# Performance work log

Hardware: AMD Instinct MI355X
Metric: run time of the kernel (lower is better)

## Reference

```python
import jax, jax.numpy as jnp
import numpy as np

B, O, L, T = 1024, 50, 20, 10
D, H, V = 64, 128, 49688
DM, FF = 2 * H, 4 * H  # transformer d_model=256, ffn=512


def _ln(x, g, b, eps=1e-5):
    m = x.mean(-1, keepdims=True)
    v = ((x - m) ** 2).mean(-1, keepdims=True)
    return (x - m) / jnp.sqrt(v + eps) * g + b


def _mha(x, in_w, in_b, out_w, out_b, nh):
    # x: [..., S, d]; torch nn.MultiheadAttention with packed qkv in_proj
    lead, S, d = x.shape[:-2], x.shape[-2], x.shape[-1]
    hd = d // nh
    qkv = x @ in_w.T + in_b
    q, k, v = jnp.split(qkv, 3, axis=-1)
    q = q.reshape(*lead, S, nh, hd)
    k = k.reshape(*lead, S, nh, hd)
    v = v.reshape(*lead, S, nh, hd)
    sc = jnp.einsum('...qhd,...khd->...hqk', q, k) / jnp.sqrt(jnp.asarray(hd, x.dtype))
    a = jax.nn.softmax(sc, axis=-1)
    o = jnp.einsum('...hqk,...khd->...qhd', a, v).reshape(*lead, S, d)
    return o @ out_w.T + out_b


def _gru_dir(x_seq, wi, wh, bi, bh):
    # x_seq: [O, B, D] -> outputs [O, B, H]; PyTorch GRU cell equations
    def step(h, x):
        gi = x @ wi.T + bi
        gh = h @ wh.T + bh
        i_r, i_z, i_n = jnp.split(gi, 3, axis=-1)
        h_r, h_z, h_n = jnp.split(gh, 3, axis=-1)
        r = jax.nn.sigmoid(i_r + h_r)
        z = jax.nn.sigmoid(i_z + h_z)
        n = jnp.tanh(i_n + r * h_n)
        h2 = (1.0 - z) * n + z * h
        return h2, h2
    h0 = jnp.zeros((x_seq.shape[1], wh.shape[1]), x_seq.dtype)
    _, ys = jax.lax.scan(step, h0, x_seq)
    return ys


def setup_inputs() -> dict:
    key = jax.random.key(0)
    ks = jax.random.split(key, 20)
    rn = lambda k, shape: jax.random.normal(k, shape, jnp.float32) * 0.05
    return {
        'order_history': jax.random.randint(ks[0], (B, O, L), 0, V, jnp.int32),
        'days_between': jax.random.uniform(ks[1], (B, T), jnp.float32) * 30.0,
        'days_since_last': jax.random.uniform(ks[2], (B,), jnp.float32) * 30.0,
        'item_emb': rn(ks[3], (V + 1, D)).at[0].set(0.0),  # padding_idx=0
        'ia_in_w': rn(ks[4], (3 * D, D)), 'ia_in_b': jnp.zeros(3 * D),
        'ia_out_w': rn(ks[5], (D, D)), 'ia_out_b': jnp.zeros(D),
        'gf_wi': rn(ks[6], (3 * H, D)), 'gf_wh': rn(ks[7], (3 * H, H)),
        'gf_bi': jnp.zeros(3 * H), 'gf_bh': jnp.zeros(3 * H),
        'gb_wi': rn(ks[8], (3 * H, D)), 'gb_wh': rn(ks[9], (3 * H, H)),
        'gb_bi': jnp.zeros(3 * H), 'gb_bh': jnp.zeros(3 * H),
        'ta_in_w': rn(ks[10], (3 * DM, DM)), 'ta_in_b': jnp.zeros(3 * DM),
        'ta_out_w': rn(ks[11], (DM, DM)), 'ta_out_b': jnp.zeros(DM),
        't_ln1_g': jnp.ones(DM), 't_ln1_b': jnp.zeros(DM),
        't_ln2_g': jnp.ones(DM), 't_ln2_b': jnp.zeros(DM),
        't_ff1_w': rn(ks[12], (FF, DM)), 't_ff1_b': jnp.zeros(FF),
        't_ff2_w': rn(ks[13], (DM, FF)), 't_ff2_b': jnp.zeros(DM),
        'te1_w': rn(ks[14], (H // 4, 2)), 'te1_b': jnp.zeros(H // 4),
        'te_ln1_g': jnp.ones(H // 4), 'te_ln1_b': jnp.zeros(H // 4),
        'te2_w': rn(ks[15], (H // 2, H // 4)), 'te2_b': jnp.zeros(H // 2),
        'te_ln2_g': jnp.ones(H // 2), 'te_ln2_b': jnp.zeros(H // 2),
        'c_w': rn(ks[16], (H, DM + H // 2)), 'c_b': jnp.zeros(H),
        'c_ln_g': jnp.ones(H), 'c_ln_b': jnp.zeros(H),
    }


def reference(order_history, days_between, days_since_last, item_emb,
              ia_in_w, ia_in_b, ia_out_w, ia_out_b,
              gf_wi, gf_wh, gf_bi, gf_bh, gb_wi, gb_wh, gb_bi, gb_bh,
              ta_in_w, ta_in_b, ta_out_w, ta_out_b,
              t_ln1_g, t_ln1_b, t_ln2_g, t_ln2_b,
              t_ff1_w, t_ff1_b, t_ff2_w, t_ff2_b,
              te1_w, te1_b, te_ln1_g, te_ln1_b, te2_w, te2_b, te_ln2_g, te_ln2_b,
              c_w, c_b, c_ln_g, c_ln_b):
    # per-order item embedding + self-attention + mean pool (batched over B,O)
    E = item_emb[order_history]                            # [B,O,L,D]
    A = _mha(E, ia_in_w, ia_in_b, ia_out_w, ia_out_b, 4)   # [B,O,L,D]
    order_emb = A.mean(axis=2)                             # [B,O,D]
    # bidirectional GRU over order sequence
    x = jnp.transpose(order_emb, (1, 0, 2))                # [O,B,D]
    yf = _gru_dir(x, gf_wi, gf_wh, gf_bi, gf_bh)
    yb = _gru_dir(x[::-1], gb_wi, gb_wh, gb_bi, gb_bh)[::-1]
    g = jnp.transpose(jnp.concatenate([yf, yb], axis=-1), (1, 0, 2))  # [B,O,2H]
    # post-norm TransformerEncoderLayer (dropout inactive at eval)
    sa = _mha(g, ta_in_w, ta_in_b, ta_out_w, ta_out_b, 4)
    h1 = _ln(g + sa, t_ln1_g, t_ln1_b)
    ff = jax.nn.relu(h1 @ t_ff1_w.T + t_ff1_b) @ t_ff2_w.T + t_ff2_b
    h2 = _ln(h1 + ff, t_ln2_g, t_ln2_b)
    order_enc = h2.mean(axis=1)                            # [B,2H]
    # temporal features: mean(days_between), recency (days_std is unused in original)
    feat = jnp.stack([days_between.mean(axis=1), days_since_last], axis=1)  # [B,2]
    t1 = jax.nn.relu(_ln(feat @ te1_w.T + te1_b, te_ln1_g, te_ln1_b))
    t2 = jax.nn.relu(_ln(t1 @ te2_w.T + te2_b, te_ln2_g, te_ln2_b))        # [B,H//2]
    u = jnp.concatenate([order_enc, t2], axis=1)           # [B,2H+H//2]
    return jax.nn.relu(_ln(u @ c_w.T + c_b, c_ln_g, c_ln_b))  # [B,H]
```

## Files before the change

### kernel.cpp

```cpp
#include <hip/hip_runtime.h>


#define B_ 1024
#define O_ 50
#define VROWS 49689
#define VPAD  49792

typedef __attribute__((ext_vector_type(8))) short  short8v;
typedef __attribute__((ext_vector_type(4))) short  short4v;
typedef __attribute__((ext_vector_type(8))) unsigned short ushort8v;
typedef __attribute__((ext_vector_type(4))) unsigned short ushort4v;
typedef __attribute__((ext_vector_type(4))) float f32x4;

__device__ __forceinline__ float sig_(float x)  { return 1.0f / (1.0f + __expf(-x)); }
__device__ __forceinline__ float tanh_(float x) { return 2.0f / (1.0f + __expf(-2.0f * x)) - 1.0f; }

__device__ __forceinline__ unsigned short f2bf(float f) {
  union { float f; unsigned int u; } v; v.f = f;
  unsigned int r = v.u + 0x7FFFu + ((v.u >> 16) & 1u);
  return (unsigned short)(r >> 16);
}
__device__ __forceinline__ float bf2f(unsigned short u) {
  union { unsigned int u; float f; } v; v.u = ((unsigned int)u) << 16;
  return v.f;
}
__device__ __forceinline__ unsigned int pk2bf(float lo, float hi) {
  return (unsigned int)f2bf(lo) | ((unsigned int)f2bf(hi) << 16);
}

struct CvArgs {
  const float* src[10];
  unsigned short* dst[10];
  int n[10];
};
__global__ void k_cv_multi(CvArgs a) {
  int i = blockIdx.x * 256 + threadIdx.x;
#pragma unroll
  for (int s = 0; s < 10; ++s) {
    if (i < a.n[s]) { a.dst[s][i] = f2bf(a.src[s][i]); return; }
    i -= a.n[s];
  }
}

__global__ void k_prep_small(const float* __restrict__ c_w, float* __restrict__ w_c,
                             const float* __restrict__ bia, const float* __restrict__ bib,
                             float* __restrict__ biascat,
                             const float* __restrict__ qb, float* __restrict__ biasq,
                             unsigned short* __restrict__ wpad) {
  int i = blockIdx.x * 256 + threadIdx.x;
  if (i < 40960) {
    int r = i / 320, c = i - r * 320;
    w_c[c * 128 + r] = c_w[i];
    return;
  }
  i -= 40960;
  if (i < 768) { biascat[i] = (i < 384) ? bia[i] : bib[i - 384]; return; }
  i -= 768;
  if (i < 256) { biasq[i] = (i < 192) ? qb[i] : 0.f; return; }
  i -= 256;
  if (i < 4096) wpad[i] = 0;
}

template<int RELU>
__global__ __launch_bounds__(256) void k_gemm128(
    const unsigned short* __restrict__ A, int lda,
    const unsigned short* __restrict__ W, int K,
    const float* __restrict__ bias,
    unsigned short* __restrict__ C, int ldc, int Mclamp)
{
  __shared__ unsigned short As[128 * 40];
  __shared__ unsigned short Bs[128 * 40];
  int n0 = blockIdx.x * 128, m0 = blockIdx.y * 128;
  int t = threadIdx.x, wv = t >> 6, lane = t & 63;
  int fr = lane & 15, kg = lane >> 4;
  int wr = wv >> 1, wc = wv & 1;
  int sr = t >> 1, sc = (t & 1) * 16;

  f32x4 acc[4][4];
#pragma unroll
  for (int mi = 0; mi < 4; ++mi)
#pragma unroll
    for (int ni = 0; ni < 4; ++ni) acc[mi][ni] = (f32x4){0.f, 0.f, 0.f, 0.f};

  int arow = m0 + sr; if (arow >= Mclamp) arow = Mclamp - 1;
  const unsigned short* ga = &A[(size_t)arow * lda + sc];
  const unsigned short* gw = &W[(size_t)(n0 + sr) * K + sc];

  for (int k0 = 0; k0 < K; k0 += 32) {
    ushort8v a0 = *(const ushort8v*)(ga + k0);
    ushort8v a1 = *(const ushort8v*)(ga + k0 + 8);
    ushort8v b0 = *(const ushort8v*)(gw + k0);
    ushort8v b1 = *(const ushort8v*)(gw + k0 + 8);
    __syncthreads();
    *(ushort8v*)&As[sr * 40 + sc]     = a0;
    *(ushort8v*)&As[sr * 40 + sc + 8] = a1;
    *(ushort8v*)&Bs[sr * 40 + sc]     = b0;
    *(ushort8v*)&Bs[sr * 40 + sc + 8] = b1;
    __syncthreads();
    short8v af[4], bfv[4];
#pragma unroll
    for (int mi = 0; mi < 4; ++mi)
      af[mi] = *(const short8v*)&As[(wr * 64 + mi * 16 + fr) * 40 + kg * 8];
#pragma unroll
    for (int ni = 0; ni < 4; ++ni)
      bfv[ni] = *(const short8v*)&Bs[(wc * 64 + ni * 16 + fr) * 40 + kg * 8];
#pragma unroll
    for (int mi = 0; mi < 4; ++mi)
#pragma unroll
      for (int ni = 0; ni < 4; ++ni)
        acc[mi][ni] = __builtin_amdgcn_mfma_f32_16x16x32_bf16(af[mi], bfv[ni], acc[mi][ni], 0, 0, 0);
  }

#pragma unroll
  for (int ni = 0; ni < 4; ++ni) {
    int col = n0 + wc * 64 + ni * 16 + fr;
    float bb = bias[col];
#pragma unroll
    for (int mi = 0; mi < 4; ++mi) {
#pragma unroll
      for (int r = 0; r < 4; ++r) {
        int row = m0 + wr * 64 + mi * 16 + kg * 4 + r;
        float v = acc[mi][ni][r] + bb;
        if (RELU) v = fmaxf(v, 0.f);
        C[(size_t)row * ldc + col] = f2bf(v);
      }
    }
  }
}

__global__ __launch_bounds__(256) void k_item_fused(
    const int* __restrict__ oh,
    const unsigned short* __restrict__ QKVall ,
    const float* __restrict__ wo , const float* __restrict__ bob,
    unsigned short* __restrict__ X )
{
  __shared__ __align__(16) unsigned short QKs[2][20][144];
  __shared__ __align__(16) unsigned short VTs[2][64][36];
  __shared__ __align__(16) unsigned short Ps[4][24][36];
  __shared__ __align__(16) float mAs[2][68];
  __shared__ int ids[2][20];

  int t = threadIdx.x, wv = t >> 6, lane = t & 63;
  int fr = lane & 15, lg = lane >> 4;
  int pr = wv >> 1, half = wv & 1;
  unsigned short (*Vs)[20][72] = (unsigned short (*)[20][72])&Ps[0][0][0];

  if (t < 40) ids[t / 20][t % 20] = oh[(size_t)(blockIdx.x * 2 + t / 20) * 20 + (t % 20)];
  {
    unsigned int* vz = (unsigned int*)&VTs[t >> 7][(t >> 1) & 63][20 + (t & 1) * 8];
    vz[0] = 0; vz[1] = 0; vz[2] = 0; vz[3] = 0;
  }
  __syncthreads();

  for (int e = t; e < 640; e += 256) {
    int pp = e / 320, rem = e - pp * 320;
    int row = rem >> 4, ch = (rem & 15) * 8;
    const unsigned short* src = QKVall + (size_t)ids[pp][row] * 256 + ch;
    *(ushort8v*)&QKs[pp][row][ch] = *(const ushort8v*)src;
  }
  for (int e = t; e < 320; e += 256) {
    int pp = e / 160, rem = e - pp * 160;
    int row = rem >> 3, ch = (rem & 7) * 8;
    const unsigned short* src = QKVall + (size_t)ids[pp][row] * 256 + 128 + ch;
    *(ushort8v*)&Vs[pp][row][ch] = *(const ushort8v*)src;
  }
  __syncthreads();

  for (int e = t; e < 640; e += 256) {
    int pp = e / 320, rem = e - pp * 320;
    int jp = rem >> 5, c0 = (rem & 31) * 2;
    unsigned int a = *(const unsigned int*)&Vs[pp][2 * jp][c0];
    unsigned int b = *(const unsigned int*)&Vs[pp][2 * jp + 1][c0];
    *(unsigned int*)&VTs[pp][c0][2 * jp]     = (a & 0xFFFFu) | (b << 16);
    *(unsigned int*)&VTs[pp][c0 + 1][2 * jp] = (a >> 16) | (b & 0xFFFF0000u);
  }
  __syncthreads();

  for (int e = lane; e < 72; e += 64) {
    int row = 20 + e / 18, col = (e - (e / 18) * 18) * 2;
    *(unsigned int*)&Ps[wv][row][col] = 0;
  }

  int rj1 = (fr + 16 < 20) ? fr + 16 : 19;
  bool iv1 = fr < 4;
  int pr1 = iv1 ? 16 + fr : 20;
#pragma unroll
  for (int hi = 0; hi < 2; ++hi) {
    int h = half * 2 + hi;
    short8v aK0, aK1, bQ0, bQ1;
    {
      short8v z = {0,0,0,0,0,0,0,0};
      aK0 = z; aK1 = z; bQ0 = z; bQ1 = z;
    }
    if (lg < 2) {
      aK0 = *(const short8v*)&QKs[pr][fr][64 + h * 16 + lg * 8];
      aK1 = *(const short8v*)&QKs[pr][rj1][64 + h * 16 + lg * 8];
      bQ0 = *(const short8v*)&QKs[pr][fr][h * 16 + lg * 8];
      bQ1 = *(const short8v*)&QKs[pr][rj1][h * 16 + lg * 8];
    }
    f32x4 s00 = {0.f,0.f,0.f,0.f}, s01 = {0.f,0.f,0.f,0.f};
    f32x4 s10 = {0.f,0.f,0.f,0.f}, s11 = {0.f,0.f,0.f,0.f};
    s00 = __builtin_amdgcn_mfma_f32_16x16x32_bf16(aK0, bQ0, s00, 0, 0, 0);
    s01 = __builtin_amdgcn_mfma_f32_16x16x32_bf16(aK0, bQ1, s01, 0, 0, 0);
    s10 = __builtin_amdgcn_mfma_f32_16x16x32_bf16(aK1, bQ0, s10, 0, 0, 0);
    s11 = __builtin_amdgcn_mfma_f32_16x16x32_bf16(aK1, bQ1, s11, 0, 0, 0);

    float e00[4], e01[4], e10[4], e11[4];
    float d0 = 0.f, d1 = 0.f;
#pragma unroll
    for (int r = 0; r < 4; ++r) {
      int j1 = 16 + lg * 4 + r;
      bool jv1 = j1 < 20;
      float v00 = __expf(0.25f * s00[r]);
      float v01 = iv1 ? __expf(0.25f * s01[r]) : 0.f;
      float v10 = jv1 ? __expf(0.25f * s10[r]) : 0.f;
      float v11 = (jv1 && iv1) ? __expf(0.25f * s11[r]) : 0.f;
      e00[r] = v00; e01[r] = v01; e10[r] = v10; e11[r] = v11;
      d0 += v00 + v10; d1 += v01 + v11;
    }
    d0 += __shfl_xor(d0, 16, 64); d0 += __shfl_xor(d0, 32, 64);
    d1 += __shfl_xor(d1, 16, 64); d1 += __shfl_xor(d1, 32, 64);
    float inv0 = __fdividef(1.f, d0);
    float inv1 = iv1 ? __fdividef(1.f, d1) : 0.f;

    *(unsigned int*)&Ps[wv][fr][lg * 4]          = pk2bf(e00[0]*inv0, e00[1]*inv0);
    *(unsigned int*)&Ps[wv][fr][lg * 4 + 2]      = pk2bf(e00[2]*inv0, e00[3]*inv0);
    *(unsigned int*)&Ps[wv][fr][16 + lg * 4]     = pk2bf(e10[0]*inv0, e10[1]*inv0);
    *(unsigned int*)&Ps[wv][fr][16 + lg * 4 + 2] = pk2bf(e10[2]*inv0, e10[3]*inv0);
    if (iv1) {
      *(unsigned int*)&Ps[wv][16 + fr][lg * 4]          = pk2bf(e01[0]*inv1, e01[1]*inv1);
      *(unsigned int*)&Ps[wv][16 + fr][lg * 4 + 2]      = pk2bf(e01[2]*inv1, e01[3]*inv1);
      *(unsigned int*)&Ps[wv][16 + fr][16 + lg * 4]     = pk2bf(e11[0]*inv1, e11[1]*inv1);
      *(unsigned int*)&Ps[wv][16 + fr][16 + lg * 4 + 2] = pk2bf(e11[2]*inv1, e11[3]*inv1);
    }

    short8v pa0, pa1, bV;
    {
      short4v l0 = *(const short4v*)&Ps[wv][fr][lg * 8];
      short4v h0 = *(const short4v*)&Ps[wv][fr][lg * 8 + 4];
      short4v l1 = *(const short4v*)&Ps[wv][pr1][lg * 8];
      short4v h1 = *(const short4v*)&Ps[wv][pr1][lg * 8 + 4];
      short4v lv = *(const short4v*)&VTs[pr][h * 16 + fr][lg * 8];
      short4v hv = *(const short4v*)&VTs[pr][h * 16 + fr][lg * 8 + 4];
      pa0[0]=l0[0]; pa0[1]=l0[1]; pa0[2]=l0[2]; pa0[3]=l0[3];
      pa0[4]=h0[0]; pa0[5]=h0[1]; pa0[6]=h0[2]; pa0[7]=h0[3];
      pa1[0]=l1[0]; pa1[1]=l1[1]; pa1[2]=l1[2]; pa1[3]=l1[3];
      pa1[4]=h1[0]; pa1[5]=h1[1]; pa1[6]=h1[2]; pa1[7]=h1[3];
      bV[0]=lv[0]; bV[1]=lv[1]; bV[2]=lv[2]; bV[3]=lv[3];
      bV[4]=hv[0]; bV[5]=hv[1]; bV[6]=hv[2]; bV[7]=hv[3];
    }
    f32x4 m20 = {0.f,0.f,0.f,0.f}, m21 = {0.f,0.f,0.f,0.f};
    m20 = __builtin_amdgcn_mfma_f32_16x16x32_bf16(pa0, bV, m20, 0, 0, 0);
    m21 = __builtin_amdgcn_mfma_f32_16x16x32_bf16(pa1, bV, m21, 0, 0, 0);

    float sm = m20[0] + m20[1] + m20[2] + m20[3];
    if (lg == 0) sm += m21[0] + m21[1] + m21[2] + m21[3];
    sm += __shfl_xor(sm, 16, 64);
    sm += __shfl_xor(sm, 32, 64);
    if (lg == 0) mAs[pr][h * 16 + fr] = sm * 0.05f;
  }
  __syncthreads();

  if (t < 128) {
    int p2 = t >> 6, col = t & 63;
    float acc = bob[col];
    const float* wrow = &wo[(size_t)col * 64];
    for (int k = 0; k < 64; k += 4) {
      float4 m4 = *(const float4*)&mAs[p2][k];
      float4 w4 = *(const float4*)(wrow + k);
      acc += m4.x * w4.x + m4.y * w4.y + m4.z * w4.z + m4.w * w4.w;
    }
    X[(size_t)(blockIdx.x * 2 + p2) * 64 + col] = f2bf(acc);
  }
}

__global__ __launch_bounds__(512) void k_gru_mfma(
    const unsigned short* __restrict__ GI,
    const unsigned short* __restrict__ whf,
    const unsigned short* __restrict__ whb,
    const float* __restrict__ bh_f, const float* __restrict__ bh_b,
    unsigned short* __restrict__ G )
{
  __shared__ unsigned short hsb[16][136];
  __shared__ float ah[4][392];

  int bid = blockIdx.x;
  int dir = bid >> 8;
  int rg  = bid & 255;
  const unsigned short* wh = dir ? whb : whf;
  const float* bh = dir ? bh_b : bh_f;

  int t = threadIdx.x;
  int w = t >> 6, lane = t & 63;
  int fr = lane & 15, kg = lane >> 4;

  short8v bfr[3][4];
#pragma unroll
  for (int n = 0; n < 3; ++n)
#pragma unroll
    for (int kf = 0; kf < 4; ++kf)
      bfr[n][kf] = *(const short8v*)&wh[(size_t)(w * 48 + n * 16 + fr) * 128 + kf * 32 + kg * 8];

  for (int e = t; e < 16 * 136; e += 512) ((unsigned short*)hsb)[e] = 0;

  int grow = t >> 7, gc = t & 127;
  float bh0 = bh[gc], bh1 = bh[128 + gc], bh2 = bh[256 + gc];
  float hold = 0.f;
  const unsigned short* gip = &GI[(size_t)(rg * 4 + grow) * 50 * 768 + dir * 384];
  unsigned short* gout = &G[((size_t)(rg * 4 + grow) * 50) * 256 + dir * 128 + gc];

  __syncthreads();

  int o0 = dir ? 49 : 0;
  unsigned short c0v = gip[(size_t)o0 * 768 + gc];
  unsigned short c1v = gip[(size_t)o0 * 768 + 128 + gc];
  unsigned short c2v = gip[(size_t)o0 * 768 + 256 + gc];

  for (int s = 0; s < 50; ++s) {
    int o  = dir ? 49 - s : s;
    unsigned short n0v = 0, n1v = 0, n2v = 0;
    if (s < 49) {
      int on = dir ? 48 - s : s + 1;
      n0v = gip[(size_t)on * 768 + gc];
      n1v = gip[(size_t)on * 768 + 128 + gc];
      n2v = gip[(size_t)on * 768 + 256 + gc];
    }

    short8v a0 = *(const short8v*)&hsb[fr][0 * 32 + kg * 8];
    short8v a1 = *(const short8v*)&hsb[fr][1 * 32 + kg * 8];
    short8v a2 = *(const short8v*)&hsb[fr][2 * 32 + kg * 8];
    short8v a3 = *(const short8v*)&hsb[fr][3 * 32 + kg * 8];

    f32x4 acc0 = {0.f,0.f,0.f,0.f}, acc1 = {0.f,0.f,0.f,0.f}, acc2 = {0.f,0.f,0.f,0.f};
    acc0 = __builtin_amdgcn_mfma_f32_16x16x32_bf16(a0, bfr[0][0], acc0, 0, 0, 0);
    acc1 = __builtin_amdgcn_mfma_f32_16x16x32_bf16(a0, bfr[1][0], acc1, 0, 0, 0);
    acc2 = __builtin_amdgcn_mfma_f32_16x16x32_bf16(a0, bfr[2][0], acc2, 0, 0, 0);
    acc0 = __builtin_amdgcn_mfma_f32_16x16x32_bf16(a1, bfr[0][1], acc0, 0, 0, 0);
    acc1 = __builtin_amdgcn_mfma_f32_16x16x32_bf16(a1, bfr[1][1], acc1, 0, 0, 0);
    acc2 = __builtin_amdgcn_mfma_f32_16x16x32_bf16(a1, bfr[2][1], acc2, 0, 0, 0);
    acc0 = __builtin_amdgcn_mfma_f32_16x16x32_bf16(a2, bfr[0][2], acc0, 0, 0, 0);
    acc1 = __builtin_amdgcn_mfma_f32_16x16x32_bf16(a2, bfr[1][2], acc1, 0, 0, 0);
    acc2 = __builtin_amdgcn_mfma_f32_16x16x32_bf16(a2, bfr[2][2], acc2, 0, 0, 0);
    acc0 = __builtin_amdgcn_mfma_f32_16x16x32_bf16(a3, bfr[0][3], acc0, 0, 0, 0);
    acc1 = __builtin_amdgcn_mfma_f32_16x16x32_bf16(a3, bfr[1][3], acc1, 0, 0, 0);
    acc2 = __builtin_amdgcn_mfma_f32_16x16x32_bf16(a3, bfr[2][3], acc2, 0, 0, 0);

    if (kg == 0) {
#pragma unroll
      for (int r = 0; r < 4; ++r) {
        ah[r][w * 48 + 0 * 16 + fr] = acc0[r];
        ah[r][w * 48 + 1 * 16 + fr] = acc1[r];
        ah[r][w * 48 + 2 * 16 + fr] = acc2[r];
      }
    }
    __syncthreads();

    float ai0 = bf2f(c0v), ai1 = bf2f(c1v), ai2 = bf2f(c2v);
    float ah0 = ah[grow][gc] + bh0;
    float ah1 = ah[grow][128 + gc] + bh1;
    float ah2 = ah[grow][256 + gc] + bh2;
    float rr = sig_(ai0 + ah0);
    float zz = sig_(ai1 + ah1);
    float nn = tanh_(ai2 + rr * ah2);
    float h2 = (1.f - zz) * nn + zz * hold;
    hold = h2;
    unsigned short hb = f2bf(h2);
    hsb[grow][gc] = hb;
    gout[(size_t)o * 256] = hb;
    c0v = n0v; c1v = n1v; c2v = n2v;
    __syncthreads();
  }
}

__global__ __launch_bounds__(256) void k_attn_core(unsigned short* __restrict__ BIG)
{
  __shared__ __align__(16) float qs[50][68], ks[50][68], vs[50][68];
  __shared__ float P[50][52];
  int bl = blockIdx.x >> 2, h = blockIdx.x & 3;
  int t = threadIdx.x;
  size_t base = (size_t)bl * 50 * 768;
  int hc = h * 64;

  for (int e = t; e < 800; e += 256) {
    int row = e >> 4, c4 = (e & 15) * 4;
    ushort4v q4 = *(const ushort4v*)&BIG[base + (size_t)row * 768 + hc + c4];
    ushort4v k4 = *(const ushort4v*)&BIG[base + (size_t)row * 768 + 256 + hc + c4];
    ushort4v v4 = *(const ushort4v*)&BIG[base + (size_t)row * 768 + 512 + hc + c4];
#pragma unroll
    for (int j = 0; j < 4; ++j) {
      qs[row][c4 + j] = bf2f(q4[j]);
      ks[row][c4 + j] = bf2f(k4[j]);
      vs[row][c4 + j] = bf2f(v4[j]);
    }
  }
  __syncthreads();

  for (int e = t; e < 2500; e += 256) {
    int i = e / 50, j = e - (e / 50) * 50;
    float d = 0.f;
#pragma unroll
    for (int k = 0; k < 64; k += 4) {
      float4 q = *(const float4*)&qs[i][k];
      float4 kk = *(const float4*)&ks[j][k];
      d += q.x * kk.x + q.y * kk.y + q.z * kk.z + q.w * kk.w;
    }
    P[i][j] = d * 0.125f;
  }
  __syncthreads();

  {
    int l = t & 31, rslot = t >> 5;
    for (int i0 = 0; i0 < 50; i0 += 8) {
      int i = i0 + rslot;
      if (i < 50) {
        float p1 = P[i][l];
        float p2 = (l < 18) ? P[i][l + 32] : -1e30f;
        float m = fmaxf(p1, p2);
#pragma unroll
        for (int d2 = 1; d2 < 32; d2 <<= 1) m = fmaxf(m, __shfl_xor(m, d2, 32));
        float e1 = __expf(p1 - m);
        float e2 = (l < 18) ? __expf(p2 - m) : 0.f;
        float s = e1 + e2;
#pragma unroll
        for (int d2 = 1; d2 < 32; d2 <<= 1) s += __shfl_xor(s, d2, 32);
        float inv = __fdividef(1.f, s);
        P[i][l] = e1 * inv;
        if (l < 18) P[i][l + 32] = e2 * inv;
      }
    }
  }
  __syncthreads();
  for (int e = t; e < 1600; e += 256) {
    int i = e >> 5, c2 = (e & 31) * 2;
    float a0 = 0.f, a1 = 0.f;
    for (int j = 0; j < 50; ++j) {
      float pv = P[i][j];
      a0 += pv * vs[j][c2];
      a1 += pv * vs[j][c2 + 1];
    }
    *(unsigned int*)&BIG[base + (size_t)i * 768 + hc + c2] = pk2bf(a0, a1);
  }
}

__global__ __launch_bounds__(256) void k_ln_res(
    const unsigned short* __restrict__ res, const unsigned short* __restrict__ add,
    int addld, unsigned short* __restrict__ dst,
    const float* __restrict__ g, const float* __restrict__ bt)
{
  int row = blockIdx.x * 4 + (threadIdx.x >> 6);
  int lane = threadIdx.x & 63;
  int c = lane * 4;
  ushort4v rv = *(const ushort4v*)&res[(size_t)row * 256 + c];
  ushort4v av = *(const ushort4v*)&add[(size_t)row * addld + c];
  float x0 = bf2f(rv[0]) + bf2f(av[0]);
  float x1 = bf2f(rv[1]) + bf2f(av[1]);
  float x2 = bf2f(rv[2]) + bf2f(av[2]);
  float x3 = bf2f(rv[3]) + bf2f(av[3]);
  float s = x0 + x1 + x2 + x3;
  float sq = x0 * x0 + x1 * x1 + x2 * x2 + x3 * x3;
#pragma unroll
  for (int d = 1; d < 64; d <<= 1) { s += __shfl_xor(s, d, 64); sq += __shfl_xor(sq, d, 64); }
  float m = s * (1.f / 256.f);
  float var = sq * (1.f / 256.f) - m * m;
  float rs = rsqrtf(var + 1e-5f);
  float4 gv = *(const float4*)&g[c];
  float4 bv = *(const float4*)&bt[c];
  ushort4v ov;
  ov[0] = f2bf((x0 - m) * rs * gv.x + bv.x);
  ov[1] = f2bf((x1 - m) * rs * gv.y + bv.y);
  ov[2] = f2bf((x2 - m) * rs * gv.z + bv.z);
  ov[3] = f2bf((x3 - m) * rs * gv.w + bv.w);
  *(ushort4v*)&dst[(size_t)row * 256 + c] = ov;
}

__global__ __launch_bounds__(256) void k_heads(
    const unsigned short* __restrict__ H2 ,
    const float* __restrict__ daysb, const float* __restrict__ dayss,
    const float* __restrict__ te1_w, const float* __restrict__ te1_b,
    const float* __restrict__ ln1g, const float* __restrict__ ln1b,
    const float* __restrict__ te2_w, const float* __restrict__ te2_b,
    const float* __restrict__ ln2g, const float* __restrict__ ln2b,
    const float* __restrict__ cWT ,
    const float* __restrict__ c_b, const float* __restrict__ clng,
    const float* __restrict__ clnb, float* __restrict__ out)
{
  __shared__ float oe[256];
  __shared__ float feat[2];
  __shared__ float s1[32], s2[64], pre[128], stat[2];
  int b = blockIdx.x, t = threadIdx.x;
  {
    float s = 0.f;
    for (int o = 0; o < 50; ++o) s += bf2f(H2[((size_t)b * 50 + o) * 256 + t]);
    oe[t] = s * 0.02f;
  }
  if (t == 0) {
    float f0 = 0.f;
    for (int i = 0; i < 10; ++i) f0 += daysb[b * 10 + i];
    feat[0] = f0 * 0.1f;
    feat[1] = dayss[b];
  }
  __syncthreads();
  if (t < 32) s1[t] = te1_b[t] + feat[0] * te1_w[2 * t] + feat[1] * te1_w[2 * t + 1];
  __syncthreads();
  if (t == 0) {
    float s = 0.f; for (int j = 0; j < 32; ++j) s += s1[j];
    float m = s * (1.f / 32.f);
    float v = 0.f; for (int j = 0; j < 32; ++j) { float d = s1[j] - m; v += d * d; }
    stat[0] = m; stat[1] = rsqrtf(v * (1.f / 32.f) + 1e-5f);
  }
  __syncthreads();
  if (t < 32) s1[t] = fmaxf((s1[t] - stat[0]) * stat[1] * ln1g[t] + ln1b[t], 0.f);
  __syncthreads();
  if (t < 64) {
    float a = te2_b[t];
    for (int k = 0; k < 32; ++k) a += s1[k] * te2_w[t * 32 + k];
    s2[t] = a;
  }
  __syncthreads();
  if (t == 0) {
    float s = 0.f; for (int j = 0; j < 64; ++j) s += s2[j];
    float m = s * (1.f / 64.f);
    float v = 0.f; for (int j = 0; j < 64; ++j) { float d = s2[j] - m; v += d * d; }
    stat[0] = m; stat[1] = rsqrtf(v * (1.f / 64.f) + 1e-5f);
  }
  __syncthreads();
  if (t < 64) s2[t] = fmaxf((s2[t] - stat[0]) * stat[1] * ln2g[t] + ln2b[t], 0.f);
  __syncthreads();
  if (t < 128) {
    float p = c_b[t];
    for (int k = 0; k < 256; ++k) p += oe[k] * cWT[k * 128 + t];
    for (int k = 0; k < 64; ++k)  p += s2[k] * cWT[(256 + k) * 128 + t];
    pre[t] = p;
  }
  __syncthreads();
  if (t == 0) {
    float s = 0.f; for (int j = 0; j < 128; ++j) s += pre[j];
    float m = s * (1.f / 128.f);
    float v = 0.f; for (int j = 0; j < 128; ++j) { float d = pre[j] - m; v += d * d; }
    stat[0] = m; stat[1] = rsqrtf(v * (1.f / 128.f) + 1e-5f);
  }
  __syncthreads();
  if (t < 128)
    out[(size_t)b * 128 + t] = fmaxf((pre[t] - stat[0]) * stat[1] * clng[t] + clnb[t], 0.f);
}

extern "C" void kernel_launch(void* const* d_in, const int* in_sizes, int n_in,
                              void* d_out, int out_size, void* d_ws, size_t ws_size,
                              hipStream_t stream)
{
  const int*   oh       = (const int*)d_in[0];
  const float* daysb    = (const float*)d_in[1];
  const float* dayss    = (const float*)d_in[2];
  const float* emb      = (const float*)d_in[3];
  const float* ia_in_w  = (const float*)d_in[4];
  const float* ia_in_b  = (const float*)d_in[5];
  const float* ia_out_w = (const float*)d_in[6];
  const float* ia_out_b = (const float*)d_in[7];
  const float* gf_wi = (const float*)d_in[8];
  const float* gf_wh = (const float*)d_in[9];
  const float* gf_bi = (const float*)d_in[10];
  const float* gf_bh = (const float*)d_in[11];
  const float* gb_wi = (const float*)d_in[12];
  const float* gb_wh = (const float*)d_in[13];
  const float* gb_bi = (const float*)d_in[14];
  const float* gb_bh = (const float*)d_in[15];
  const float* ta_in_w  = (const float*)d_in[16];
  const float* ta_in_b  = (const float*)d_in[17];
  const float* ta_out_w = (const float*)d_in[18];
  const float* ta_out_b = (const float*)d_in[19];
  const float* t_ln1_g = (const float*)d_in[20];
  const float* t_ln1_b = (const float*)d_in[21];
  const float* t_ln2_g = (const float*)d_in[22];
  const float* t_ln2_b = (const float*)d_in[23];
  const float* t_ff1_w = (const float*)d_in[24];
  const float* t_ff1_b = (const float*)d_in[25];
  const float* t_ff2_w = (const float*)d_in[26];
  const float* t_ff2_b = (const float*)d_in[27];
  const float* te1_w = (const float*)d_in[28];
  const float* te1_b = (const float*)d_in[29];
  const float* te_ln1_g = (const float*)d_in[30];
  const float* te_ln1_b = (const float*)d_in[31];
  const float* te2_w = (const float*)d_in[32];
  const float* te2_b = (const float*)d_in[33];
  const float* te_ln2_g = (const float*)d_in[34];
  const float* te_ln2_b = (const float*)d_in[35];
  const float* c_w   = (const float*)d_in[36];
  const float* c_b   = (const float*)d_in[37];
  const float* c_ln_g = (const float*)d_in[38];
  const float* c_ln_b = (const float*)d_in[39];

  float* ws = (float*)d_ws;
  const size_t OFF_GB   = 0;
  const size_t OFF_X    = 6553600;
  const size_t OFF_S    = OFF_X + 1638400;
  const size_t OW_C     = OFF_S + 19660800;
  const size_t OW_BC    = OW_C + 40960;
  const size_t OW_BQ    = OW_BC + 768;
  const size_t OW_BF    = OW_BQ + 256;
  const size_t OW_EMB   = OW_BF + 344064;
  const size_t TOTAL    = OW_EMB + 1590048;
  if (ws_size < TOTAL * sizeof(float)) return;

  unsigned short* Gb = (unsigned short*)(ws + OFF_GB);
  unsigned short* Xb = (unsigned short*)(ws + OFF_X);
  float* w_c  = ws + OW_C;
  float* biascat = ws + OW_BC;
  float* biasq   = ws + OW_BQ;
  unsigned short* bfp = (unsigned short*)(ws + OW_BF);
  unsigned short* b_ta_in  = bfp;
  unsigned short* b_ta_out = b_ta_in + 196608;
  unsigned short* b_ff1    = b_ta_out + 65536;
  unsigned short* b_ff2    = b_ff1 + 131072;
  unsigned short* b_qkvw   = b_ff2 + 131072;
  unsigned short* b_wi_f   = b_qkvw + 16384;
  unsigned short* b_wi_b   = b_wi_f + 24576;
  unsigned short* b_wh_f   = b_wi_b + 24576;
  unsigned short* b_wh_b   = b_wh_f + 49152;
  unsigned short* embb = (unsigned short*)(ws + OW_EMB);

  unsigned short* QKVall = (unsigned short*)(ws + OFF_S);
  unsigned short* GI     = (unsigned short*)(ws + OFF_S);
  unsigned short* BIGb   = (unsigned short*)(ws + OFF_S);

  k_prep_small<<<(40960 + 768 + 256 + 4096 + 255) / 256, 256, 0, stream>>>(
      c_w, w_c, gf_bi, gb_bi, biascat, ia_in_b, biasq, b_qkvw + 12288);
  {
    CvArgs a;
    a.src[0] = ta_in_w;  a.dst[0] = b_ta_in;  a.n[0] = 196608;
    a.src[1] = ta_out_w; a.dst[1] = b_ta_out; a.n[1] = 65536;
    a.src[2] = t_ff1_w;  a.dst[2] = b_ff1;    a.n[2] = 131072;
    a.src[3] = t_ff2_w;  a.dst[3] = b_ff2;    a.n[3] = 131072;
    a.src[4] = ia_in_w;  a.dst[4] = b_qkvw;   a.n[4] = 12288;
    a.src[5] = gf_wi;    a.dst[5] = b_wi_f;   a.n[5] = 24576;
    a.src[6] = gb_wi;    a.dst[6] = b_wi_b;   a.n[6] = 24576;
    a.src[7] = gf_wh;    a.dst[7] = b_wh_f;   a.n[7] = 49152;
    a.src[8] = gb_wh;    a.dst[8] = b_wh_b;   a.n[8] = 49152;
    a.src[9] = emb;      a.dst[9] = embb;     a.n[9] = 3180096;
    int total = 196608 + 65536 + 131072 + 131072 + 12288 + 24576 + 24576 + 49152 + 49152 + 3180096;
    k_cv_multi<<<(total + 255) / 256, 256, 0, stream>>>(a);
  }

  k_gemm128<0><<<dim3(256 / 128, VPAD / 128), 256, 0, stream>>>(
      embb, 64, b_qkvw, 64, biasq, QKVall, 256, VROWS);

  k_item_fused<<<B_ * O_ / 2, 256, 0, stream>>>(oh, QKVall, ia_out_w, ia_out_b, Xb);

  k_gemm128<0><<<dim3(768 / 128, 51200 / 128), 256, 0, stream>>>(
      Xb, 64, b_wi_f , 64, biascat, GI, 768, 51200);
  k_gru_mfma<<<512, 512, 0, stream>>>(GI, b_wh_f, b_wh_b, gf_bh, gb_bh, Gb);

  k_gemm128<0><<<dim3(768 / 128, 51200 / 128), 256, 0, stream>>>(
      Gb, 256, b_ta_in, 256, ta_in_b, BIGb, 768, 51200);
  k_attn_core<<<B_ * 4, 256, 0, stream>>>(BIGb);
  k_gemm128<0><<<dim3(256 / 128, 51200 / 128), 256, 0, stream>>>(
      BIGb, 768, b_ta_out, 256, ta_out_b, BIGb + 256, 768, 51200);
  k_ln_res<<<51200 / 4, 256, 0, stream>>>(Gb, BIGb + 256, 768, Gb, t_ln1_g, t_ln1_b);
  k_gemm128<1><<<dim3(512 / 128, 51200 / 128), 256, 0, stream>>>(
      Gb, 256, b_ff1, 256, t_ff1_b, BIGb, 768, 51200);
  k_gemm128<0><<<dim3(256 / 128, 51200 / 128), 256, 0, stream>>>(
      BIGb, 768, b_ff2, 512, t_ff2_b, BIGb + 512, 768, 51200);
  k_ln_res<<<51200 / 4, 256, 0, stream>>>(Gb, BIGb + 512, 768, Gb, t_ln2_g, t_ln2_b);

  k_heads<<<B_, 256, 0, stream>>>(Gb, daysb, dayss, te1_w, te1_b, te_ln1_g, te_ln1_b,
                                  te2_w, te2_b, te_ln2_g, te_ln2_b,
                                  w_c, c_b, c_ln_g, c_ln_b, (float*)d_out);
}
```

Baseline: 576.9 us.

## Rewrite per-head attention core with bf16 MFMA for QK^T and PV

Replaces the scalar fp32 LDS-based attention (dot products, shared-memory softmax, scalar PV) with bf16 MFMA 16x16x32 instructions. Each wave handles 16 query rows, keeps scores in registers, does the softmax with cross-lane shuffles, writes normalized probabilities as bf16 to LDS, and uses a transposed V tile for the second MFMA. Sequences are padded from 50 to 64 with zeroed rows and keys masked. This cuts ALU work and LDS traffic, but rounds the probabilities to bf16 and adds a transpose step plus extra barriers.

```diff
diff --git a/kernel.cpp b/kernel.cpp
--- a/kernel.cpp
+++ b/kernel.cpp
@@ -374,71 +374,115 @@
 
 __global__ __launch_bounds__(256) void k_attn_core(unsigned short* __restrict__ BIG)
 {
-  __shared__ __align__(16) float qs[50][68], ks[50][68], vs[50][68];
-  __shared__ float P[50][52];
+  __shared__ __align__(16) unsigned short Qs[64][72];
+  __shared__ __align__(16) unsigned short Ks[64][72];
+  __shared__ __align__(16) unsigned short VTs[64][72];
+  __shared__ __align__(16) unsigned short Ps[4][16][72];
+  unsigned short (*Vs)[64] = (unsigned short (*)[64])&Ps[0][0][0];
+
   int bl = blockIdx.x >> 2, h = blockIdx.x & 3;
-  int t = threadIdx.x;
+  int t = threadIdx.x, wv = t >> 6, lane = t & 63;
+  int fr = lane & 15, lg = lane >> 4;
   size_t base = (size_t)bl * 50 * 768;
   int hc = h * 64;
 
+  for (int e = t; e < 504; e += 256) {
+    int r = e / 36, c = (e - r * 36) * 2;
+    *(unsigned int*)&Qs[50 + r][c] = 0;
+    *(unsigned int*)&Ks[50 + r][c] = 0;
+  }
+  for (int e = t; e < 2304; e += 256) {
+    int r = e / 36, c = (e - r * 36) * 2;
+    *(unsigned int*)&VTs[r][c] = 0;
+  }
+  __syncthreads();
+
+  for (int e = t; e < 400; e += 256) {
+    int row = e >> 3, ch = (e & 7) * 8;
+    *(ushort8v*)&Qs[row][ch] = *(const ushort8v*)&BIG[base + (size_t)row * 768 + hc + ch];
+  }
+  for (int e = t; e < 400; e += 256) {
+    int row = e >> 3, ch = (e & 7) * 8;
+    *(ushort8v*)&Ks[row][ch] = *(const ushort8v*)&BIG[base + (size_t)row * 768 + 256 + hc + ch];
+  }
+  for (int e = t; e < 400; e += 256) {
+    int row = e >> 3, ch = (e & 7) * 8;
+    *(ushort8v*)&Vs[row][ch] = *(const ushort8v*)&BIG[base + (size_t)row * 768 + 512 + hc + ch];
+  }
+  __syncthreads();
+
   for (int e = t; e < 800; e += 256) {
-    int row = e >> 4, c4 = (e & 15) * 4;
-    ushort4v q4 = *(const ushort4v*)&BIG[base + (size_t)row * 768 + hc + c4];
-    ushort4v k4 = *(const ushort4v*)&BIG[base + (size_t)row * 768 + 256 + hc + c4];
-    ushort4v v4 = *(const ushort4v*)&BIG[base + (size_t)row * 768 + 512 + hc + c4];
-#pragma unroll
-    for (int j = 0; j < 4; ++j) {
-      qs[row][c4 + j] = bf2f(q4[j]);
-      ks[row][c4 + j] = bf2f(k4[j]);
-      vs[row][c4 + j] = bf2f(v4[j]);
-    }
-  }
-  __syncthreads();
-
-  for (int e = t; e < 2500; e += 256) {
-    int i = e / 50, j = e - (e / 50) * 50;
-    float d = 0.f;
-#pragma unroll
-    for (int k = 0; k < 64; k += 4) {
-      float4 q = *(const float4*)&qs[i][k];
-      float4 kk = *(const float4*)&ks[j][k];
-      d += q.x * kk.x + q.y * kk.y + q.z * kk.z + q.w * kk.w;
-    }
-    P[i][j] = d * 0.125f;
-  }
-  __syncthreads();
-
-  {
-    int l = t & 31, rslot = t >> 5;
-    for (int i0 = 0; i0 < 50; i0 += 8) {
-      int i = i0 + rslot;
-      if (i < 50) {
-        float p1 = P[i][l];
-        float p2 = (l < 18) ? P[i][l + 32] : -1e30f;
-        float m = fmaxf(p1, p2);
-#pragma unroll
-        for (int d2 = 1; d2 < 32; d2 <<= 1) m = fmaxf(m, __shfl_xor(m, d2, 32));
-        float e1 = __expf(p1 - m);
-        float e2 = (l < 18) ? __expf(p2 - m) : 0.f;
-        float s = e1 + e2;
-#pragma unroll
-        for (int d2 = 1; d2 < 32; d2 <<= 1) s += __shfl_xor(s, d2, 32);
-        float inv = __fdividef(1.f, s);
-        P[i][l] = e1 * inv;
-        if (l < 18) P[i][l + 32] = e2 * inv;
-      }
-    }
-  }
-  __syncthreads();
-  for (int e = t; e < 1600; e += 256) {
-    int i = e >> 5, c2 = (e & 31) * 2;
-    float a0 = 0.f, a1 = 0.f;
-    for (int j = 0; j < 50; ++j) {
-      float pv = P[i][j];
-      a0 += pv * vs[j][c2];
-      a1 += pv * vs[j][c2 + 1];
-    }
-    *(unsigned int*)&BIG[base + (size_t)i * 768 + hc + c2] = pk2bf(a0, a1);
+    int jp = e >> 5, c0 = (e & 31) * 2;
+    unsigned int a = *(const unsigned int*)&Vs[2 * jp][c0];
+    unsigned int b = *(const unsigned int*)&Vs[2 * jp + 1][c0];
+    *(unsigned int*)&VTs[c0][2 * jp]     = (a & 0xFFFFu) | (b << 16);
+    *(unsigned int*)&VTs[c0 + 1][2 * jp] = (a >> 16) | (b & 0xFFFF0000u);
+  }
+  __syncthreads();
+
+  int i0 = wv * 16;
+  short8v bQ0 = *(const short8v*)&Qs[i0 + fr][lg * 8];
+  short8v bQ1 = *(const short8v*)&Qs[i0 + fr][32 + lg * 8];
+
+  f32x4 s[4];
+#pragma unroll
+  for (int jt = 0; jt < 4; ++jt) {
+    short8v aK0 = *(const short8v*)&Ks[jt * 16 + fr][lg * 8];
+    short8v aK1 = *(const short8v*)&Ks[jt * 16 + fr][32 + lg * 8];
+    f32x4 acc = {0.f, 0.f, 0.f, 0.f};
+    acc = __builtin_amdgcn_mfma_f32_16x16x32_bf16(aK0, bQ0, acc, 0, 0, 0);
+    acc = __builtin_amdgcn_mfma_f32_16x16x32_bf16(aK1, bQ1, acc, 0, 0, 0);
+    s[jt] = acc;
+  }
+
+  float m = -1e30f;
+#pragma unroll
+  for (int jt = 0; jt < 4; ++jt)
+#pragma unroll
+    for (int r = 0; r < 4; ++r) {
+      int j = jt * 16 + lg * 4 + r;
+      float v = s[jt][r] * 0.125f;
+      if (j < 50) m = fmaxf(m, v);
+    }
+  m = fmaxf(m, __shfl_xor(m, 16, 64));
+  m = fmaxf(m, __shfl_xor(m, 32, 64));
+
+  float ev[4][4];
+  float den = 0.f;
+#pragma unroll
+  for (int jt = 0; jt < 4; ++jt)
+#pragma unroll
+    for (int r = 0; r < 4; ++r) {
+      int j = jt * 16 + lg * 4 + r;
+      float e = (j < 50) ? __expf(s[jt][r] * 0.125f - m) : 0.f;
+      ev[jt][r] = e;
+      den += e;
+    }
+  den += __shfl_xor(den, 16, 64);
+  den += __shfl_xor(den, 32, 64);
+  float inv = __fdividef(1.f, den);
+
+#pragma unroll
+  for (int jt = 0; jt < 4; ++jt) {
+    *(unsigned int*)&Ps[wv][fr][jt * 16 + lg * 4]     = pk2bf(ev[jt][0] * inv, ev[jt][1] * inv);
+    *(unsigned int*)&Ps[wv][fr][jt * 16 + lg * 4 + 2] = pk2bf(ev[jt][2] * inv, ev[jt][3] * inv);
+  }
+
+  short8v pa0 = *(const short8v*)&Ps[wv][fr][lg * 8];
+  short8v pa1 = *(const short8v*)&Ps[wv][fr][32 + lg * 8];
+#pragma unroll
+  for (int dt = 0; dt < 4; ++dt) {
+    short8v bV0 = *(const short8v*)&VTs[dt * 16 + fr][lg * 8];
+    short8v bV1 = *(const short8v*)&VTs[dt * 16 + fr][32 + lg * 8];
+    f32x4 o = {0.f, 0.f, 0.f, 0.f};
+    o = __builtin_amdgcn_mfma_f32_16x16x32_bf16(pa0, bV0, o, 0, 0, 0);
+    o = __builtin_amdgcn_mfma_f32_16x16x32_bf16(pa1, bV1, o, 0, 0, 0);
+#pragma unroll
+    for (int r = 0; r < 4; ++r) {
+      int i = i0 + lg * 4 + r;
+      if (i < 50)
+        BIG[base + (size_t)i * 768 + hc + dt * 16 + fr] = f2bf(o[r]);
+    }
   }
 }
 
```

New measurement: 516.5 us. 1.12x faster.
